# Optimization experiments

Measured on AMD Instinct MI355X. Metric: run time of the kernel, lower is better.

The kernel has to match this reference:

```python
import jax, jax.numpy as jnp
import numpy as np

WIN = 20        # unfold kernel_size
STRIDE = 10     # window_size // 2
EPS = 1e-5


def _patches(x):
    """x: [B, H, W] -> [B, n_windows, WIN*WIN] (im2col, stride=STRIDE, VALID)."""
    p = jax.lax.conv_general_dilated_patches(
        x[:, None, :, :], (WIN, WIN), (STRIDE, STRIDE), 'VALID')
    B = x.shape[0]
    return jnp.transpose(p.reshape(B, WIN * WIN, -1), (0, 2, 1))


def _ssq_error(c, e, m):
    """Scale-invariant SSQ error per batch element. c,e,m: [B, nW, P]."""
    v = jnp.sum(e * e * m, axis=2)            # [B, nW]
    a = jnp.sum(c * e * m, axis=2)            # [B, nW]
    safe_v = jnp.where(v > EPS, v, 1.0)
    alpha = jnp.where(v > EPS, a / safe_v, 0.0)
    r = c - alpha[:, :, None] * e
    ssq = jnp.sum(m * r * r, axis=(1, 2))     # [B]
    total = jnp.sum(m * c * c, axis=(1, 2))   # [B]
    return ssq / total


def setup_inputs() -> dict:
    key = jax.random.key(0)
    k1, k2, k3 = jax.random.split(key, 3)
    B, C, H, W = 16, 3, 512, 512
    correct = jax.random.uniform(k1, (B, C, H, W), dtype=jnp.float32)
    estimate = jax.random.uniform(k2, (B, C, H, W), dtype=jnp.float32)
    mask = jax.random.uniform(k3, (B, C, H, W), dtype=jnp.float32)
    return {"correct": correct, "estimate": estimate, "mask": mask}


def reference(correct, estimate, mask):
    err = jnp.zeros((correct.shape[0],), dtype=correct.dtype)
    for ch in range(3):  # fixed small channel loop, as in the original
        err = err + _ssq_error(_patches(correct[:, ch]),
                               _patches(estimate[:, ch]),
                               _patches(mask[:, ch]))
    return jnp.mean(err) / 3.0
```

## Files before the change

### kernel.cpp

```cpp
#include <hip/hip_runtime.h>
#include <hip/hip_bf16.h>

#define HWDIM 512
#define NWIN 50
#define NT 51
#define NBC 48
#define NSTRIPE (NBC * NT)
#define EPSV 1e-5f

typedef float f32x4 __attribute__((ext_vector_type(4)));


__global__ __launch_bounds__(256) void tile_kernel(const float* __restrict__ C,
                                                   const float* __restrict__ E,
                                                   const float* __restrict__ M,
                                                   float4* __restrict__ tiles4,
                                                   int* __restrict__ cnt) {
    int t = threadIdx.x;
    if (blockIdx.x == 0 && t == 0) *cnt = 0;

    int blk   = blockIdx.x;
    int plane = blk / NT;
    int ty    = blk % NT;
    int c4    = t & 127;
    int rh    = t >> 7;
    bool isf2 = ((c4 % 5) == 2);

    size_t base = ((size_t)plane * HWDIM + (size_t)ty * 10 + rh) * HWDIM + 4 * c4;

    f32x4 cv[5], ev[5], mv[5];
    #pragma unroll
    for (int it = 0; it < 5; ++it) {
        const float* pc = C + base + (size_t)(2 * it) * HWDIM;
        const float* pe = E + base + (size_t)(2 * it) * HWDIM;
        const float* pm = M + base + (size_t)(2 * it) * HWDIM;
        asm volatile("global_load_dwordx4 %0, %1, off" : "=v"(cv[it]) : "v"(pc));
        asm volatile("global_load_dwordx4 %0, %1, off" : "=v"(ev[it]) : "v"(pe));
        asm volatile("global_load_dwordx4 %0, %1, off" : "=v"(mv[it]) : "v"(pm));
    }
    asm volatile("s_waitcnt vmcnt(0)" ::: "memory");
    __builtin_amdgcn_sched_barrier(0);

    float s01[3] = {0.f, 0.f, 0.f};
    float s23[3] = {0.f, 0.f, 0.f};
    #pragma unroll
    for (int it = 0; it < 5; ++it) {
        f32x4 c = cv[it], e = ev[it], m = mv[it];
        float mcx = m.x * c.x, mcy = m.y * c.y, mcz = m.z * c.z, mcw = m.w * c.w;
        float mex = m.x * e.x, mey = m.y * e.y, mez = m.z * e.z, mew = m.w * e.w;
        s01[0] = fmaf(mcx, c.x, s01[0]); s01[0] = fmaf(mcy, c.y, s01[0]);
        s01[1] = fmaf(mcx, e.x, s01[1]); s01[1] = fmaf(mcy, e.y, s01[1]);
        s01[2] = fmaf(mex, e.x, s01[2]); s01[2] = fmaf(mey, e.y, s01[2]);
        s23[0] = fmaf(mcz, c.z, s23[0]); s23[0] = fmaf(mcw, c.w, s23[0]);
        s23[1] = fmaf(mcz, e.z, s23[1]); s23[1] = fmaf(mcw, e.w, s23[1]);
        s23[2] = fmaf(mez, e.z, s23[2]); s23[2] = fmaf(mew, e.w, s23[2]);
    }

    __shared__ float lds[256 * 6];
    #pragma unroll
    for (int comp = 0; comp < 3; ++comp) {
        float lo = s01[comp] + (isf2 ? 0.f : s23[comp]);
        float hi = isf2 ? s23[comp] : 0.f;
        lds[t * 6 + comp]     = lo;
        lds[t * 6 + 3 + comp] = hi;
    }
    __syncthreads();

    if (t < NT) {
        int tx = t;
        int k  = tx >> 1;
        float sums[3];
        #pragma unroll
        for (int comp = 0; comp < 3; ++comp) {
            float s;
            if ((tx & 1) == 0) {
                int b = 5 * k;
                s = lds[b * 6 + comp] + lds[(b + 1) * 6 + comp] + lds[(b + 2) * 6 + comp]
                  + lds[(b + 128) * 6 + comp] + lds[(b + 129) * 6 + comp] + lds[(b + 130) * 6 + comp];
            } else {
                int b = 5 * k + 2;
                s = lds[b * 6 + 3 + comp] + lds[(b + 1) * 6 + comp] + lds[(b + 2) * 6 + comp]
                  + lds[(b + 128) * 6 + 3 + comp] + lds[(b + 129) * 6 + comp] + lds[(b + 130) * 6 + comp];
            }
            sums[comp] = s;
        }
        tiles4[(size_t)blk * NT + tx] = make_float4(sums[0], sums[1], sums[2], 0.f);
    }
}

__global__ __launch_bounds__(256) void window_final_kernel(const float4* __restrict__ tiles4,
                                                           float* __restrict__ acc,
                                                           int* __restrict__ cnt,
                                                           float* __restrict__ out) {
    int plane = blockIdx.x;
    int t     = threadIdx.x;

    __shared__ float4 lt[NT * NT];
    const float4* tp4 = tiles4 + (size_t)plane * NT * NT;
    #pragma unroll
    for (int k = 0; k < 11; ++k) {
        int i = t + k * 256;
        if (i < NT * NT) lt[i] = tp4[i];
    }
    __syncthreads();

    float ssq = 0.0f, tot = 0.0f;
    #pragma unroll
    for (int k = 0; k < 10; ++k) {
        int w = t + k * 256;
        if (w < NWIN * NWIN) {
            int wy = w / NWIN, wx = w % NWIN;
            float4 a = lt[wy * NT + wx];
            float4 b = lt[wy * NT + wx + 1];
            float4 c = lt[(wy + 1) * NT + wx];
            float4 d = lt[(wy + 1) * NT + wx + 1];
            float s_cc = a.x + b.x + c.x + d.x;
            float s_ce = a.y + b.y + c.y + d.y;
            float s_ee = a.z + b.z + c.z + d.z;
            float a2v = (s_ee > EPSV) ? (s_ce * s_ce / s_ee) : 0.0f;
            ssq += s_cc - a2v;
            tot += s_cc;
        }
    }

    #pragma unroll
    for (int d = 1; d < 64; d <<= 1) {
        ssq += __shfl_xor(ssq, d);
        tot += __shfl_xor(tot, d);
    }
    __shared__ float sr[8];
    __shared__ int   sflag;
    int lane = t & 63, wave = t >> 6;
    if (lane == 0) { sr[wave] = ssq; sr[4 + wave] = tot; }
    __syncthreads();

    if (t == 0) {
        float S = sr[0] + sr[1] + sr[2] + sr[3];
        float T = sr[4] + sr[5] + sr[6] + sr[7];
        acc[plane] = S / T;
        __threadfence();
        sflag = (atomicAdd(cnt, 1) == NBC - 1);
    }
    __syncthreads();
    if (!sflag) return;

    __threadfence();
    if (t < 64) {
        float r = (t < NBC) ? *(volatile const float*)(acc + t) : 0.0f;
        #pragma unroll
        for (int d = 1; d < 64; d <<= 1) r += __shfl_xor(r, d);
        if (t == 0) out[0] = r / (float)NBC;
    }
}

extern "C" void kernel_launch(void* const* d_in, const int* in_sizes, int n_in,
                              void* d_out, int out_size, void* d_ws, size_t ws_size,
                              hipStream_t stream) {
    const float* correct  = (const float*)d_in[0];
    const float* estimate = (const float*)d_in[1];
    const float* mask     = (const float*)d_in[2];
    float* out = (float*)d_out;

    int*    cnt    = (int*)d_ws;
    float*  acc    = (float*)d_ws + 64;
    float4* tiles4 = (float4*)((float*)d_ws + 128);

    tile_kernel<<<NSTRIPE, 256, 0, stream>>>(correct, estimate, mask, tiles4, cnt);
    window_final_kernel<<<NBC, 256, 0, stream>>>(tiles4, acc, cnt, out);
}
```

Baseline: 37.05 us.

## Fuse tile and window kernels via per-plane last-block atomic counters

Merges the tile-sum and window/final kernels into one launch. The last tile block of each plane, detected with a per-plane atomic counter, does that plane's window reduction, and a second counter picks the final block. A small zero kernel now resets the counters, and the inline-asm loads are replaced with plain float4 loads. This removes the second kernel's dependent launch and lets plane reductions overlap remaining tile work, at the cost of relaxed atomic stores and loads plus the extra zero-kernel launch.

```diff
diff --git a/kernel.cpp b/kernel.cpp
--- a/kernel.cpp
+++ b/kernel.cpp
@@ -8,17 +8,22 @@
 #define NSTRIPE (NBC * NT)
 #define EPSV 1e-5f
 
-typedef float f32x4 __attribute__((ext_vector_type(4)));
 
+union F2U { float2 f; unsigned long long u; };
 
-__global__ __launch_bounds__(256) void tile_kernel(const float* __restrict__ C,
-                                                   const float* __restrict__ E,
-                                                   const float* __restrict__ M,
-                                                   float4* __restrict__ tiles4,
-                                                   int* __restrict__ cnt) {
+__global__ void zero_kernel(int* cnt) {
     int t = threadIdx.x;
-    if (blockIdx.x == 0 && t == 0) *cnt = 0;
+    if (t < NBC + 1) cnt[t] = 0;
+}
 
+__global__ __launch_bounds__(256) void fused_kernel(const float* __restrict__ C,
+                                                    const float* __restrict__ E,
+                                                    const float* __restrict__ M,
+                                                    float4* __restrict__ tiles4,
+                                                    int* __restrict__ cnt,
+                                                    float* __restrict__ acc,
+                                                    float* __restrict__ out) {
+    int t     = threadIdx.x;
     int blk   = blockIdx.x;
     int plane = blk / NT;
     int ty    = blk % NT;
@@ -28,24 +33,20 @@
 
     size_t base = ((size_t)plane * HWDIM + (size_t)ty * 10 + rh) * HWDIM + 4 * c4;
 
-    f32x4 cv[5], ev[5], mv[5];
+    float4 cv[5], ev[5], mv[5];
     #pragma unroll
     for (int it = 0; it < 5; ++it) {
-        const float* pc = C + base + (size_t)(2 * it) * HWDIM;
-        const float* pe = E + base + (size_t)(2 * it) * HWDIM;
-        const float* pm = M + base + (size_t)(2 * it) * HWDIM;
-        asm volatile("global_load_dwordx4 %0, %1, off" : "=v"(cv[it]) : "v"(pc));
-        asm volatile("global_load_dwordx4 %0, %1, off" : "=v"(ev[it]) : "v"(pe));
-        asm volatile("global_load_dwordx4 %0, %1, off" : "=v"(mv[it]) : "v"(pm));
+        size_t o = base + (size_t)(2 * it) * HWDIM;
+        cv[it] = *(const float4*)(C + o);
+        ev[it] = *(const float4*)(E + o);
+        mv[it] = *(const float4*)(M + o);
     }
-    asm volatile("s_waitcnt vmcnt(0)" ::: "memory");
-    __builtin_amdgcn_sched_barrier(0);
 
     float s01[3] = {0.f, 0.f, 0.f};
     float s23[3] = {0.f, 0.f, 0.f};
     #pragma unroll
     for (int it = 0; it < 5; ++it) {
-        f32x4 c = cv[it], e = ev[it], m = mv[it];
+        float4 c = cv[it], e = ev[it], m = mv[it];
         float mcx = m.x * c.x, mcy = m.y * c.y, mcz = m.z * c.z, mcw = m.w * c.w;
         float mex = m.x * e.x, mey = m.y * e.y, mez = m.z * e.z, mew = m.w * e.w;
         s01[0] = fmaf(mcx, c.x, s01[0]); s01[0] = fmaf(mcy, c.y, s01[0]);
@@ -84,23 +85,35 @@
             }
             sums[comp] = s;
         }
-        tiles4[(size_t)blk * NT + tx] = make_float4(sums[0], sums[1], sums[2], 0.f);
+        F2U lo, hi;
+        lo.f = make_float2(sums[0], sums[1]);
+        hi.f = make_float2(sums[2], 0.f);
+        unsigned long long* p = (unsigned long long*)&tiles4[(size_t)blk * NT + tx];
+        __hip_atomic_store(p,     lo.u, __ATOMIC_RELAXED, __HIP_MEMORY_SCOPE_AGENT);
+        __hip_atomic_store(p + 1, hi.u, __ATOMIC_RELAXED, __HIP_MEMORY_SCOPE_AGENT);
     }
-}
+    asm volatile("s_waitcnt vmcnt(0)" ::: "memory");
+    __syncthreads();
 
-__global__ __launch_bounds__(256) void window_final_kernel(const float4* __restrict__ tiles4,
-                                                           float* __restrict__ acc,
-                                                           int* __restrict__ cnt,
-                                                           float* __restrict__ out) {
-    int plane = blockIdx.x;
-    int t     = threadIdx.x;
+    __shared__ int sflag;
+    if (t == 0)
+        sflag = (__hip_atomic_fetch_add(&cnt[plane], 1, __ATOMIC_RELAXED,
+                                        __HIP_MEMORY_SCOPE_AGENT) == NT - 1);
+    __syncthreads();
+    if (!sflag) return;
 
     __shared__ float4 lt[NT * NT];
-    const float4* tp4 = tiles4 + (size_t)plane * NT * NT;
+    const unsigned long long* tp =
+        (const unsigned long long*)(tiles4 + (size_t)plane * NT * NT);
     #pragma unroll
     for (int k = 0; k < 11; ++k) {
         int i = t + k * 256;
-        if (i < NT * NT) lt[i] = tp4[i];
+        if (i < NT * NT) {
+            F2U a, b;
+            a.u = __hip_atomic_load(tp + 2 * i,     __ATOMIC_RELAXED, __HIP_MEMORY_SCOPE_AGENT);
+            b.u = __hip_atomic_load(tp + 2 * i + 1, __ATOMIC_RELAXED, __HIP_MEMORY_SCOPE_AGENT);
+            lt[i] = make_float4(a.f.x, a.f.y, b.f.x, b.f.y);
+        }
     }
     __syncthreads();
 
@@ -129,7 +142,6 @@
         tot += __shfl_xor(tot, d);
     }
     __shared__ float sr[8];
-    __shared__ int   sflag;
     int lane = t & 63, wave = t >> 6;
     if (lane == 0) { sr[wave] = ssq; sr[4 + wave] = tot; }
     __syncthreads();
@@ -137,16 +149,18 @@
     if (t == 0) {
         float S = sr[0] + sr[1] + sr[2] + sr[3];
         float T = sr[4] + sr[5] + sr[6] + sr[7];
-        acc[plane] = S / T;
-        __threadfence();
-        sflag = (atomicAdd(cnt, 1) == NBC - 1);
+        __hip_atomic_store(&acc[plane], S / T, __ATOMIC_RELAXED, __HIP_MEMORY_SCOPE_AGENT);
+        asm volatile("s_waitcnt vmcnt(0)" ::: "memory");
+        sflag = (__hip_atomic_fetch_add(&cnt[NBC], 1, __ATOMIC_RELAXED,
+                                        __HIP_MEMORY_SCOPE_AGENT) == NBC - 1);
     }
     __syncthreads();
     if (!sflag) return;
 
-    __threadfence();
     if (t < 64) {
-        float r = (t < NBC) ? *(volatile const float*)(acc + t) : 0.0f;
+        float r = 0.0f;
+        if (t < NBC)
+            r = __hip_atomic_load(&acc[t], __ATOMIC_RELAXED, __HIP_MEMORY_SCOPE_AGENT);
         #pragma unroll
         for (int d = 1; d < 64; d <<= 1) r += __shfl_xor(r, d);
         if (t == 0) out[0] = r / (float)NBC;
@@ -165,6 +179,7 @@
     float*  acc    = (float*)d_ws + 64;
     float4* tiles4 = (float4*)((float*)d_ws + 128);
 
-    tile_kernel<<<NSTRIPE, 256, 0, stream>>>(correct, estimate, mask, tiles4, cnt);
-    window_final_kernel<<<NBC, 256, 0, stream>>>(tiles4, acc, cnt, out);
+    zero_kernel<<<1, 64, 0, stream>>>(cnt);
+    fused_kernel<<<NSTRIPE, 256, 0, stream>>>(correct, estimate, mask,
+                                              tiles4, cnt, acc, out);
 }
```

After: 51.00 us, median of 3. 1.38x slower.
